# Kernel tuning notes

Hardware: AMD Instinct MI355X
Metric: run time of the kernel (lower is better)

## Reference

```python
import jax, jax.numpy as jnp
import numpy as np
from jax import lax

# --- model constants (match init_kwargs) ---
B = 4096
T, N_FEAT = 100, 81
KH = 7                 # cnn_kernel_height
T_MOD = T - KH + 1     # 94
M = 100                # cnn_hidden_size
P = 128                # decoder hidden size
SKIP = 10
SH = 32                # skip_hidden_size
PT = T_MOD // SKIP     # 9


def setup_inputs() -> dict:
    key = jax.random.key(0)
    ks = jax.random.split(key, 18)
    s = 0.05
    def rn(k, shape, scale=s):
        return jax.random.normal(k, shape, dtype=jnp.float32) * scale
    return {
        "enc_data": jax.random.normal(ks[0], (B, T, N_FEAT), dtype=jnp.float32),
        # Conv2d(1 -> M, kernel=(KH, N_FEAT))
        "conv_w": rn(ks[1], (M, 1, KH, N_FEAT)),
        "conv_b": rn(ks[2], (M,)),
        # TemporalAttention: W_d: Linear(2P->M, no bias), U_d: Linear(M->M, no bias), v_d: Linear(M->1, no bias)
        "Wd": rn(ks[3], (M, 2 * P)),
        "Ud": rn(ks[4], (M, M)),
        "vd": rn(ks[5], (1, M)),
        # LSTM(input=M, hidden=P), PyTorch gate order i,f,g,o
        "lstm_wih": rn(ks[6], (4 * P, M)),
        "lstm_whh": rn(ks[7], (4 * P, P)),
        "lstm_bih": rn(ks[8], (4 * P,)),
        "lstm_bhh": rn(ks[9], (4 * P,)),
        # GRU(input=M, hidden=SH), PyTorch gate order r,z,n
        "gru_wih": rn(ks[10], (3 * SH, M)),
        "gru_whh": rn(ks[11], (3 * SH, SH)),
        "gru_bih": rn(ks[12], (3 * SH,)),
        "gru_bhh": rn(ks[13], (3 * SH,)),
        # output head: Linear(M+P+SKIP*SH -> P), ReLU, (Dropout=eval identity), Linear(P -> 1)
        "out1_w": rn(ks[14], (P, M + P + SKIP * SH)),
        "out1_b": rn(ks[15], (P,)),
        "out2_w": rn(ks[16], (1, P)),
        "out2_b": rn(ks[17], (1,)),
    }


def reference(enc_data, conv_w, conv_b, Wd, Ud, vd,
              lstm_wih, lstm_whh, lstm_bih, lstm_bhh,
              gru_wih, gru_whh, gru_bih, gru_bhh,
              out1_w, out1_b, out2_w, out2_b):
    b = enc_data.shape[0]

    # --- CNN encoder: Conv2d valid over full feature width -> [B, T_MOD, M] ---
    x = enc_data[:, None]  # [B,1,T,n]
    h = lax.conv_general_dilated(x, conv_w, window_strides=(1, 1), padding='VALID',
                                 dimension_numbers=('NCHW', 'OIHW', 'NCHW'))  # [B,M,T_MOD,1]
    H = jax.nn.relu(h + conv_b[None, :, None, None])[..., 0].transpose(0, 2, 1)  # [B,T_MOD,M]

    # precompute U_d(H) once (same math; U_d applied to H is step-invariant)
    HU = jnp.einsum('btm,km->btk', H, Ud)  # [B,T_MOD,M]

    def dec_step(carry, _):
        d, s = carry  # each [B,P]
        q = jnp.concatenate([d, s], axis=1)                       # [B,2P]
        e = jnp.tanh((q @ Wd.T)[:, None, :] + HU)                 # [B,T_MOD,M]
        scores = jnp.einsum('btm,m->bt', e, vd[0])                # [B,T_MOD]
        beta = jax.nn.softmax(scores, axis=1)                     # softmax over time
        c = jnp.einsum('bt,btm->bm', beta, H)                     # context [B,M]
        gates = c @ lstm_wih.T + lstm_bih + d @ lstm_whh.T + lstm_bhh
        i_g, f_g, g_g, o_g = jnp.split(gates, 4, axis=1)
        s_new = jax.nn.sigmoid(f_g) * s + jax.nn.sigmoid(i_g) * jnp.tanh(g_g)
        d_new = jax.nn.sigmoid(o_g) * jnp.tanh(s_new)
        return (d_new, s_new), (beta, c)

    d0 = jnp.zeros((b, P), dtype=enc_data.dtype)
    s0 = jnp.zeros((b, P), dtype=enc_data.dtype)
    (d_T, _), (betas, cs) = lax.scan(dec_step, (d0, s0), None, length=T_MOD)
    c_last = cs[-1]                                               # [B,M]
    dec_out = jnp.concatenate([d_T, c_last], axis=1)              # [B, P+M]

    # --- skip GRU over strided conv features ---
    Hs = H[:, -PT * SKIP:, :]                                     # [B, PT*SKIP, M]
    Hs = (Hs.transpose(0, 2, 1)                                   # [B, M, PT*SKIP]
            .reshape(b, M, PT, SKIP)
            .transpose(2, 0, 3, 1)                                # [PT, B, SKIP, M]
            .reshape(PT, b * SKIP, M))

    def gru_step(hprev, xt):
        gi = xt @ gru_wih.T + gru_bih
        gh = hprev @ gru_whh.T + gru_bhh
        ir, iz, inn = jnp.split(gi, 3, axis=1)
        hr, hz, hn = jnp.split(gh, 3, axis=1)
        r = jax.nn.sigmoid(ir + hr)
        z = jax.nn.sigmoid(iz + hz)
        nn_ = jnp.tanh(inn + r * hn)
        hnew = (1.0 - z) * nn_ + z * hprev
        return hnew, None

    h0 = jnp.zeros((b * SKIP, SH), dtype=enc_data.dtype)
    h_skip, _ = lax.scan(gru_step, h0, Hs)                        # [B*SKIP, SH]
    h_skip = h_skip.reshape(b, SKIP * SH)                         # matches torch view

    feat = jnp.concatenate([dec_out, h_skip], axis=1)             # [B, P+M+SKIP*SH]
    out = jax.nn.relu(feat @ out1_w.T + out1_b) @ out2_w.T + out2_b  # [B,1]
    return out[:, 0]
```

## Files before the change

### kernel.cpp

```cpp
#include <hip/hip_runtime.h>

typedef unsigned int u32;
typedef unsigned short u16;
typedef _Float16 half2_t __attribute__((ext_vector_type(2)));

#define TM 94
#define MD 100
#define DEC_NT 512

__device__ __forceinline__ float bf2f(u16 v){ return __builtin_bit_cast(float, ((u32)v)<<16); }
__device__ __forceinline__ float bflo(u32 v){ return __builtin_bit_cast(float, v<<16); }
__device__ __forceinline__ float bfhi(u32 v){ return __builtin_bit_cast(float, v & 0xffff0000u); }
__device__ __forceinline__ u32 f2bf_bits(float f){ u32 u=__builtin_bit_cast(u32,f); return (u + 0x7fffu + ((u>>16)&1u))>>16; }
__device__ __forceinline__ u32 packbf2(float a, float b){ return f2bf_bits(a) | (f2bf_bits(b)<<16); }
__device__ __forceinline__ u32 packh2(float a, float b){ half2_t h; h.x=(_Float16)a; h.y=(_Float16)b; return __builtin_bit_cast(u32,h); }
__device__ __forceinline__ float fdot2(u32 a, u32 b, float c){
  return __builtin_amdgcn_fdot2(__builtin_bit_cast(half2_t,a), __builtin_bit_cast(half2_t,b), c, false);
}
__device__ __forceinline__ float fast_rcp(float x){ return __builtin_amdgcn_rcpf(x); }
__device__ __forceinline__ float sigmoid_f(float x){ return fast_rcp(1.f + __expf(-x)); }
__device__ __forceinline__ float tanh_f(float x){ float e=__expf(2.f*x); return 1.f - 2.f*fast_rcp(e+1.f); }

__global__ __launch_bounds__(128)
void conv_kernel(const float* __restrict__ enc, const float* __restrict__ cw,
                 const float* __restrict__ cb, u16* __restrict__ Hb)
{
  __shared__ float sE[8100];
  const int tid = threadIdx.x;
  const int b = blockIdx.y;
  const int chunk = blockIdx.x;
  const float* ep = enc + (size_t)b*8100;
  for (int i=tid;i<8100;i+=128) sE[i]=ep[i];
  __syncthreads();
  if (tid >= TM) return;
  const int t = tid;
  const int mo = chunk*10;
  const float* wb = cw + mo*567;
  float acc[10];
  #pragma unroll
  for (int k=0;k<10;k++) acc[k]=cb[mo+k];
  const float* e = sE + t*81;
  #pragma unroll 3
  for (int j=0;j<567;j++){
    float ev = e[j];
    #pragma unroll
    for (int k=0;k<10;k++) acc[k] += ev*wb[k*567+j];
  }
  u32* out = (u32*)Hb + ((size_t)b*9400 + t*100 + mo)/2;
  #pragma unroll
  for (int k=0;k<5;k++) out[k] = packbf2(fmaxf(acc[2*k],0.f), fmaxf(acc[2*k+1],0.f));
}

#define OFF_SHU   37600
#define OFF_SQ    75200
#define OFF_SQ2   77248
#define OFF_SA    78272
#define OFF_SB    79072
#define OFF_SC    79840
#define OFF_SC2   80640
#define OFF_SG    81056
#define OFF_SVD   85152
#define DEC_LDS   85568

__global__ __launch_bounds__(DEC_NT, 2)
void decoder_kernel(const u16* __restrict__ Hb, const float* __restrict__ Wd,
                    const float* __restrict__ Ud, const float* __restrict__ vd,
                    const float* __restrict__ wih, const float* __restrict__ whh,
                    const float* __restrict__ bih, const float* __restrict__ bhh,
                    float* __restrict__ dT, float* __restrict__ cLast)
{
  extern __shared__ char smem[];
  u16*      sH   = (u16*)smem;
  u16*      sHU  = (u16*)(smem + OFF_SHU);
  float*    sq   = (float*)(smem + OFF_SQ);
  _Float16* sq2  = (_Float16*)(smem + OFF_SQ2);
  float*    sa   = (float*)(smem + OFF_SA);
  float*    sbeta= (float*)(smem + OFF_SB);
  float*    sc   = (float*)(smem + OFF_SC);
  _Float16* sc2  = (_Float16*)(smem + OFF_SC2);
  float*    sg   = (float*)(smem + OFF_SG);
  float*    svd  = (float*)(smem + OFF_SVD);

  const int tid = threadIdx.x;
  const int b0 = blockIdx.x * 2;

  {
    const u32* src = (const u32*)(Hb + (size_t)b0*9400);
    u32* dst = (u32*)sH;
    for (int i=tid;i<9400;i+=DEC_NT) dst[i]=src[i];
  }
  if (tid < 100) svd[tid] = vd[tid];
  for (int i=tid;i<512;i+=DEC_NT) sq[i]=0.f;
  {
    u32* q2 = (u32*)sq2;
    for (int i=tid;i<256;i+=DEC_NT) q2[i]=0u;
  }

  u32 Wih[50]; u32 Whh[64]; u32 Wdf[32];
  float biasg;
  {
    const float2* wr = (const float2*)(wih + (size_t)tid*100);
    #pragma unroll
    for (int i=0;i<50;i++){ float2 v = wr[i]; Wih[i]=packh2(v.x,v.y); }
    const float2* hr = (const float2*)(whh + (size_t)tid*128);
    #pragma unroll
    for (int i=0;i<64;i++){ float2 v = hr[i]; Whh[i]=packh2(v.x,v.y); }
    biasg = bih[tid] + bhh[tid];
  }
  const int mw = tid>>2, part = tid&3;
  if (mw < 100){
    const float2* dr = (const float2*)(Wd + mw*256 + part*64);
    #pragma unroll
    for (int i=0;i<32;i++){ float2 v = dr[i]; Wdf[i]=packh2(v.x,v.y); }
  }
  __syncthreads();

  for (int idx=tid; idx<4700; idx+=DEC_NT){
    int kq = idx/188;
    int r  = idx - kq*188;
    int bi = (r>=94)?1:0;
    int t  = r - 94*bi;
    const u32* hrow = (const u32*)sH + bi*4700 + t*50;
    const float* ud0 = Ud + (kq*4+0)*100;
    const float* ud1 = Ud + (kq*4+1)*100;
    const float* ud2 = Ud + (kq*4+2)*100;
    const float* ud3 = Ud + (kq*4+3)*100;
    float c0=0.f,c1=0.f,c2=0.f,c3=0.f;
    #pragma unroll 5
    for (int mq=0; mq<25; mq++){
      u32 h01 = hrow[mq*2], h23 = hrow[mq*2+1];
      float h0=bflo(h01), h1=bfhi(h01), h2=bflo(h23), h3=bfhi(h23);
      float4 u0 = *(const float4*)(ud0 + mq*4);
      float4 u1 = *(const float4*)(ud1 + mq*4);
      float4 u2 = *(const float4*)(ud2 + mq*4);
      float4 u3 = *(const float4*)(ud3 + mq*4);
      c0 += h0*u0.x + h1*u0.y + h2*u0.z + h3*u0.w;
      c1 += h0*u1.x + h1*u1.y + h2*u1.z + h3*u1.w;
      c2 += h0*u2.x + h1*u2.y + h2*u2.z + h3*u2.w;
      c3 += h0*u3.x + h1*u3.y + h2*u3.z + h3*u3.w;
    }
    u32* dst = (u32*)sHU + bi*4700 + t*50 + kq*2;
    dst[0] = packbf2(c0,c1);
    dst[1] = packbf2(c2,c3);
  }
  __syncthreads();

  for (int step=0; step<TM; step++){
    if (mw < 100){
      #pragma unroll
      for (int bi=0;bi<2;bi++){
        const uint4* qp = (const uint4*)((const u32*)sq2 + bi*128 + part*32);
        float a0=0.f, a1=0.f;
        #pragma unroll
        for (int i=0;i<8;i++){
          uint4 qv = qp[i];
          a0 = fdot2(Wdf[4*i+0], qv.x, a0);
          a1 = fdot2(Wdf[4*i+1], qv.y, a1);
          a0 = fdot2(Wdf[4*i+2], qv.z, a0);
          a1 = fdot2(Wdf[4*i+3], qv.w, a1);
        }
        float acc = a0+a1;
        acc += __shfl_xor(acc,1);
        acc += __shfl_xor(acc,2);
        if (part==0) sa[bi*100+mw]=acc;
      }
    }
    __syncthreads();
    if (tid < 376){
      int row = tid>>1, half = tid&1;
      int bi = (row>=94)?1:0;
      int t = row - 94*bi;
      const u16* hu = sHU + bi*9400 + t*100 + half*50;
      const float* ap = sa + bi*100 + half*50;
      const float* vp = svd + half*50;
      float acc=0.f;
      #pragma unroll 5
      for (int m=0;m<50;m++){
        float x = ap[m] + bf2f(hu[m]);
        acc += vp[m]*tanh_f(x);
      }
      acc += __shfl_xor(acc,1);
      if (half==0) sbeta[bi*96+t]=acc;
    }
    __syncthreads();
    if (tid < 128){
      int bi = tid>>6, lane = tid&63;
      float s0 = sbeta[bi*96+lane];
      float s1 = (lane<30)? sbeta[bi*96+64+lane] : -1e30f;
      float mx = fmaxf(s0,s1);
      #pragma unroll
      for (int o=32;o>=1;o>>=1) mx = fmaxf(mx, __shfl_xor(mx,o));
      float e0 = __expf(s0-mx);
      float e1 = (lane<30)? __expf(s1-mx) : 0.f;
      float sm = e0+e1;
      #pragma unroll
      for (int o=32;o>=1;o>>=1) sm += __shfl_xor(sm,o);
      float rs = fast_rcp(sm);
      sbeta[bi*96+lane] = e0*rs;
      if (lane<30) sbeta[bi*96+64+lane] = e1*rs;
    }
    __syncthreads();
    if (tid < 400){
      int bi = (tid>=200)?1:0;
      int rr = tid - 200*bi;
      int m = rr>>1, th = rr&1;
      const float* bp = sbeta + bi*96 + th*47;
      const u16* hp = sH + bi*9400 + th*4700 + m;
      float a0=0.f;
      #pragma unroll
      for (int i=0;i<47;i++) a0 += bp[i]*bf2f(hp[i*100]);
      a0 += __shfl_xor(a0,1);
      if (th==0){
        sc[bi*100+m]=a0;
        sc2[bi*104+m]=(_Float16)a0;
        if (step==TM-1) cLast[(size_t)(b0+bi)*100+m]=a0;
      }
    }
    __syncthreads();
    #pragma unroll
    for (int bi=0;bi<2;bi++){
      float a0 = biasg, a1 = 0.f;
      const uint4* cp = (const uint4*)((const u32*)sc2 + bi*52);
      #pragma unroll
      for (int i=0;i<12;i++){
        uint4 cv = cp[i];
        a0 = fdot2(Wih[4*i+0], cv.x, a0);
        a1 = fdot2(Wih[4*i+1], cv.y, a1);
        a0 = fdot2(Wih[4*i+2], cv.z, a0);
        a1 = fdot2(Wih[4*i+3], cv.w, a1);
      }
      {
        const u32* ct = (const u32*)sc2 + bi*52 + 48;
        a0 = fdot2(Wih[48], ct[0], a0);
        a1 = fdot2(Wih[49], ct[1], a1);
      }
      const uint4* qp = (const uint4*)((const u32*)sq2 + bi*128);
      #pragma unroll
      for (int i=0;i<16;i++){
        uint4 qv = qp[i];
        a0 = fdot2(Whh[4*i+0], qv.x, a0);
        a1 = fdot2(Whh[4*i+1], qv.y, a1);
        a0 = fdot2(Whh[4*i+2], qv.z, a0);
        a1 = fdot2(Whh[4*i+3], qv.w, a1);
      }
      sg[bi*512+tid] = a0+a1;
    }
    __syncthreads();
    if (tid < 256){
      int bi = tid>>7, p = tid&127;
      float ig = sg[bi*512+p];
      float fg = sg[bi*512+128+p];
      float gg = sg[bi*512+256+p];
      float og = sg[bi*512+384+p];
      float s_old = sq[bi*256+128+p];
      float sn = sigmoid_f(fg)*s_old + sigmoid_f(ig)*tanh_f(gg);
      float dn = sigmoid_f(og)*tanh_f(sn);
      sq[bi*256+128+p]=sn; sq[bi*256+p]=dn;
      sq2[bi*256+p]=(_Float16)dn; sq2[bi*256+128+p]=(_Float16)sn;
      if (step==TM-1) dT[(size_t)(b0+bi)*128+p]=dn;
    }
    __syncthreads();
  }
}

__global__ __launch_bounds__(256)
void gru_kernel(const u16* __restrict__ Hb, const float* __restrict__ wih,
                const float* __restrict__ whh, const float* __restrict__ bihp,
                const float* __restrict__ bhhp, float* __restrict__ hskip)
{
  __shared__ float sWih[96][101];
  __shared__ float sWhh[96][33];
  __shared__ float sxt[8][100];
  __shared__ float sh[8][33];
  const int tid = threadIdx.x;
  for (int i=tid;i<9600;i+=256){ sWih[i/100][i%100]=wih[i]; }
  for (int i=tid;i<3072;i+=256){ sWhh[i>>5][i&31]=whh[i]; }
  const int r = tid>>5, j = tid&31;
  const int rowg = blockIdx.x*8 + r;
  const int b = rowg/10, sk = rowg - b*10;
  const float b_r = bihp[j], b_z = bihp[32+j], b_n = bihp[64+j];
  const float hb_r = bhhp[j], hb_z = bhhp[32+j], hb_n = bhhp[64+j];
  sh[r][j]=0.f;
  float h = 0.f;
  __syncthreads();
  for (int pt=0; pt<9; pt++){
    for (int i=tid;i<800;i+=256){
      int rr=i/100, m=i-rr*100;
      int rg = blockIdx.x*8+rr; int bb=rg/10, ss=rg-bb*10;
      sxt[rr][m] = bf2f(Hb[(size_t)bb*9400 + (size_t)(4+pt*10+ss)*100 + m]);
    }
    __syncthreads();
    float gi_r=b_r, gi_z=b_z, gi_n=b_n, gh_r=hb_r, gh_z=hb_z, gh_n=hb_n;
    #pragma unroll 4
    for (int m=0;m<100;m++){
      float x = sxt[r][m];
      gi_r += sWih[j][m]*x; gi_z += sWih[32+j][m]*x; gi_n += sWih[64+j][m]*x;
    }
    #pragma unroll
    for (int k=0;k<32;k++){
      float hp = sh[r][k];
      gh_r += sWhh[j][k]*hp; gh_z += sWhh[32+j][k]*hp; gh_n += sWhh[64+j][k]*hp;
    }
    float rg_ = sigmoid_f(gi_r+gh_r);
    float z  = sigmoid_f(gi_z+gh_z);
    float n  = tanh_f(gi_n + rg_*gh_n);
    h = (1.f-z)*n + z*h;
    __syncthreads();
    sh[r][j]=h;
    __syncthreads();
  }
  hskip[(size_t)b*320 + sk*32 + j] = h;
}

__global__ __launch_bounds__(256)
void out_kernel(const float* __restrict__ dT, const float* __restrict__ cLast,
                const float* __restrict__ hskip, const float* __restrict__ w1,
                const float* __restrict__ b1, const float* __restrict__ w2,
                const float* __restrict__ b2, float* __restrict__ outp)
{
  __shared__ float sf[2][548];
  __shared__ float sred[2][2];
  const int tid = threadIdx.x;
  const int b0 = blockIdx.x*2;
  for (int i=tid;i<2*548;i+=256){
    int bl=i/548, k=i-548*bl; int b=b0+bl;
    float v;
    if (k<128) v = dT[(size_t)b*128+k];
    else if (k<228) v = cLast[(size_t)b*100+(k-128)];
    else v = hskip[(size_t)b*320+(k-228)];
    sf[bl][k]=v;
  }
  __syncthreads();
  const int bl = tid>>7, j = tid&127;
  const float* wr = w1 + (size_t)j*548;
  float acc = b1[j];
  #pragma unroll 4
  for (int k=0;k<548;k++) acc += sf[bl][k]*wr[k];
  float v = fmaxf(acc,0.f)*w2[j];
  #pragma unroll
  for (int o=32;o>=1;o>>=1) v += __shfl_xor(v,o);
  if ((tid&63)==0) sred[bl][j>>6]=v;
  __syncthreads();
  if (j==0) outp[b0+bl] = sred[bl][0]+sred[bl][1]+b2[0];
}

extern "C" void kernel_launch(void* const* d_in, const int* in_sizes, int n_in,
                              void* d_out, int out_size, void* d_ws, size_t ws_size,
                              hipStream_t stream)
{
  const float* enc      = (const float*)d_in[0];
  const float* conv_w   = (const float*)d_in[1];
  const float* conv_b   = (const float*)d_in[2];
  const float* Wd       = (const float*)d_in[3];
  const float* Ud       = (const float*)d_in[4];
  const float* vd       = (const float*)d_in[5];
  const float* lstm_wih = (const float*)d_in[6];
  const float* lstm_whh = (const float*)d_in[7];
  const float* lstm_bih = (const float*)d_in[8];
  const float* lstm_bhh = (const float*)d_in[9];
  const float* gru_wih  = (const float*)d_in[10];
  const float* gru_whh  = (const float*)d_in[11];
  const float* gru_bih  = (const float*)d_in[12];
  const float* gru_bhh  = (const float*)d_in[13];
  const float* out1_w   = (const float*)d_in[14];
  const float* out1_b   = (const float*)d_in[15];
  const float* out2_w   = (const float*)d_in[16];
  const float* out2_b   = (const float*)d_in[17];

  char* ws = (char*)d_ws;
  u16*   Hb    = (u16*)ws;
  float* dT    = (float*)(ws + 77004800);
  float* cLast = (float*)(ws + 79101952);
  float* hskip = (float*)(ws + 80740352);

  conv_kernel<<<dim3(10,4096,1), 128, 0, stream>>>(enc, conv_w, conv_b, Hb);

  (void)hipFuncSetAttribute((const void*)decoder_kernel,
                            hipFuncAttributeMaxDynamicSharedMemorySize, DEC_LDS);
  decoder_kernel<<<2048, DEC_NT, DEC_LDS, stream>>>(Hb, Wd, Ud, vd,
                                                    lstm_wih, lstm_whh, lstm_bih, lstm_bhh,
                                                    dT, cLast);

  gru_kernel<<<5120, 256, 0, stream>>>(Hb, gru_wih, gru_whh, gru_bih, gru_bhh, hskip);

  out_kernel<<<2048, 256, 0, stream>>>(dT, cLast, hskip, out1_w, out1_b, out2_w, out2_b,
                                       (float*)d_out);
}
```

Measured before the change: 8.196 ms.

## Process four batch items per decoder block and tile output head weights in LDS

The decoder kernel now handles four sequences per block instead of two, so the per-thread LSTM and attention weights held in registers are reused across more batch items. Several inner loops are vectorized and rebalanced: full-row tanh scoring per thread, paired context outputs, and rotated Wd reads to spread LDS bank access. Gate values are stored as fp16 and the weight register loads are moved after the Ud precompute. The output head now runs 32 batch items per block with w1 staged through LDS tiles. This raises decoder LDS use to about 163KB, which may cut occupancy to one block per CU, and the fp16 gate storage lowers precision.

```diff
diff --git a/kernel.cpp b/kernel.cpp
--- a/kernel.cpp
+++ b/kernel.cpp
@@ -5,7 +5,7 @@
 typedef _Float16 half2_t __attribute__((ext_vector_type(2)));
 
 #define TM 94
-#define MD 100
+#define NB 4
 #define DEC_NT 512
 
 __device__ __forceinline__ float bf2f(u16 v){ return __builtin_bit_cast(float, ((u32)v)<<16); }
@@ -51,16 +51,15 @@
   for (int k=0;k<5;k++) out[k] = packbf2(fmaxf(acc[2*k],0.f), fmaxf(acc[2*k+1],0.f));
 }
 
-#define OFF_SHU   37600
-#define OFF_SQ    75200
-#define OFF_SQ2   77248
-#define OFF_SA    78272
-#define OFF_SB    79072
-#define OFF_SC    79840
-#define OFF_SC2   80640
-#define OFF_SG    81056
-#define OFF_SVD   85152
-#define DEC_LDS   85568
+#define OFF_SHU   75200
+#define OFF_SQS   150400
+#define OFF_SQ2   152448
+#define OFF_SA    154496
+#define OFF_SB    156096
+#define OFF_SC2   157632
+#define OFF_SG    158464
+#define OFF_SVD   162560
+#define DEC_LDS   162960
 
 __global__ __launch_bounds__(DEC_NT, 2)
 void decoder_kernel(const u16* __restrict__ Hb, const float* __restrict__ Wd,
@@ -72,53 +71,34 @@
   extern __shared__ char smem[];
   u16*      sH   = (u16*)smem;
   u16*      sHU  = (u16*)(smem + OFF_SHU);
-  float*    sq   = (float*)(smem + OFF_SQ);
+  float*    sqs  = (float*)(smem + OFF_SQS);
   _Float16* sq2  = (_Float16*)(smem + OFF_SQ2);
   float*    sa   = (float*)(smem + OFF_SA);
   float*    sbeta= (float*)(smem + OFF_SB);
-  float*    sc   = (float*)(smem + OFF_SC);
-  _Float16* sc2  = (_Float16*)(smem + OFF_SC2);
-  float*    sg   = (float*)(smem + OFF_SG);
+  u32*      sc2  = (u32*)(smem + OFF_SC2);
+  _Float16* sg   = (_Float16*)(smem + OFF_SG);
   float*    svd  = (float*)(smem + OFF_SVD);
 
   const int tid = threadIdx.x;
-  const int b0 = blockIdx.x * 2;
+  const int b0 = blockIdx.x * NB;
 
   {
-    const u32* src = (const u32*)(Hb + (size_t)b0*9400);
-    u32* dst = (u32*)sH;
-    for (int i=tid;i<9400;i+=DEC_NT) dst[i]=src[i];
+    const uint4* src = (const uint4*)(Hb + (size_t)b0*9400);
+    uint4* dst = (uint4*)sH;
+    for (int i=tid;i<4700;i+=DEC_NT) dst[i]=src[i];
   }
   if (tid < 100) svd[tid] = vd[tid];
-  for (int i=tid;i<512;i+=DEC_NT) sq[i]=0.f;
+  for (int i=tid;i<NB*128;i+=DEC_NT) sqs[i]=0.f;
   {
     u32* q2 = (u32*)sq2;
-    for (int i=tid;i<256;i+=DEC_NT) q2[i]=0u;
-  }
-
-  u32 Wih[50]; u32 Whh[64]; u32 Wdf[32];
-  float biasg;
-  {
-    const float2* wr = (const float2*)(wih + (size_t)tid*100);
-    #pragma unroll
-    for (int i=0;i<50;i++){ float2 v = wr[i]; Wih[i]=packh2(v.x,v.y); }
-    const float2* hr = (const float2*)(whh + (size_t)tid*128);
-    #pragma unroll
-    for (int i=0;i<64;i++){ float2 v = hr[i]; Whh[i]=packh2(v.x,v.y); }
-    biasg = bih[tid] + bhh[tid];
-  }
-  const int mw = tid>>2, part = tid&3;
-  if (mw < 100){
-    const float2* dr = (const float2*)(Wd + mw*256 + part*64);
-    #pragma unroll
-    for (int i=0;i<32;i++){ float2 v = dr[i]; Wdf[i]=packh2(v.x,v.y); }
+    for (int i=tid;i<NB*128;i+=DEC_NT) q2[i]=0u;
   }
   __syncthreads();
 
-  for (int idx=tid; idx<4700; idx+=DEC_NT){
-    int kq = idx/188;
-    int r  = idx - kq*188;
-    int bi = (r>=94)?1:0;
+  for (int idx=tid; idx<9400; idx+=DEC_NT){
+    int kq = idx/376;
+    int r  = idx - kq*376;
+    int bi = r/94;
     int t  = r - 94*bi;
     const u32* hrow = (const u32*)sH + bi*4700 + t*50;
     const float* ud0 = Ud + (kq*4+0)*100;
@@ -128,8 +108,8 @@
     float c0=0.f,c1=0.f,c2=0.f,c3=0.f;
     #pragma unroll 5
     for (int mq=0; mq<25; mq++){
-      u32 h01 = hrow[mq*2], h23 = hrow[mq*2+1];
-      float h0=bflo(h01), h1=bfhi(h01), h2=bflo(h23), h3=bfhi(h23);
+      uint2 hp = *(const uint2*)(hrow + mq*2);
+      float h0=bflo(hp.x), h1=bfhi(hp.x), h2=bflo(hp.y), h3=bfhi(hp.y);
       float4 u0 = *(const float4*)(ud0 + mq*4);
       float4 u1 = *(const float4*)(ud1 + mq*4);
       float4 u2 = *(const float4*)(ud2 + mq*4);
@@ -145,19 +125,43 @@
   }
   __syncthreads();
 
+  __builtin_amdgcn_sched_barrier(0);
+  const int mw = tid>>2, part = tid&3;
+  u32 Wih[50]; u32 Whh[64]; u32 Wdf[32];
+  float biasg;
+  {
+    const float2* wr = (const float2*)(wih + (size_t)tid*100);
+    #pragma unroll
+    for (int i=0;i<50;i++){ float2 v = wr[i]; Wih[i]=packh2(v.x,v.y); }
+    const float2* hr = (const float2*)(whh + (size_t)tid*128);
+    #pragma unroll
+    for (int i=0;i<64;i++){ float2 v = hr[i]; Whh[i]=packh2(v.x,v.y); }
+    biasg = bih[tid] + bhh[tid];
+  }
+  if (mw < 100){
+    const float2* dr = (const float2*)(Wd + mw*256 + part*64);
+    #pragma unroll
+    for (int s=0;s<8;s++){
+      int ii = (s+part)&7;
+      #pragma unroll
+      for (int k=0;k<4;k++){ float2 v = dr[ii*4+k]; Wdf[4*s+k]=packh2(v.x,v.y); }
+    }
+  }
+
   for (int step=0; step<TM; step++){
     if (mw < 100){
       #pragma unroll
-      for (int bi=0;bi<2;bi++){
-        const uint4* qp = (const uint4*)((const u32*)sq2 + bi*128 + part*32);
+      for (int bi=0;bi<NB;bi++){
+        const u32* qb = (const u32*)sq2 + bi*128 + part*32;
         float a0=0.f, a1=0.f;
         #pragma unroll
-        for (int i=0;i<8;i++){
-          uint4 qv = qp[i];
-          a0 = fdot2(Wdf[4*i+0], qv.x, a0);
-          a1 = fdot2(Wdf[4*i+1], qv.y, a1);
-          a0 = fdot2(Wdf[4*i+2], qv.z, a0);
-          a1 = fdot2(Wdf[4*i+3], qv.w, a1);
+        for (int s=0;s<8;s++){
+          int ii = (s+part)&7;
+          uint4 qv = *(const uint4*)(qb + ii*4);
+          a0 = fdot2(Wdf[4*s+0], qv.x, a0);
+          a1 = fdot2(Wdf[4*s+1], qv.y, a1);
+          a0 = fdot2(Wdf[4*s+2], qv.z, a0);
+          a1 = fdot2(Wdf[4*s+3], qv.w, a1);
         }
         float acc = a0+a1;
         acc += __shfl_xor(acc,1);
@@ -167,23 +171,38 @@
     }
     __syncthreads();
     if (tid < 376){
-      int row = tid>>1, half = tid&1;
-      int bi = (row>=94)?1:0;
-      int t = row - 94*bi;
-      const u16* hu = sHU + bi*9400 + t*100 + half*50;
-      const float* ap = sa + bi*100 + half*50;
-      const float* vp = svd + half*50;
+      int bi = tid/94;
+      int t  = tid - 94*bi;
+      const u32* hu = (const u32*)sHU + bi*4700 + t*50;
+      const float4* ap4 = (const float4*)(sa + bi*100);
+      const float4* vp4 = (const float4*)svd;
       float acc=0.f;
-      #pragma unroll 5
-      for (int m=0;m<50;m++){
-        float x = ap[m] + bf2f(hu[m]);
-        acc += vp[m]*tanh_f(x);
-      }
-      acc += __shfl_xor(acc,1);
-      if (half==0) sbeta[bi*96+t]=acc;
-    }
-    __syncthreads();
-    if (tid < 128){
+      #pragma unroll
+      for (int c=0;c<12;c++){
+        uint4 h4 = ((const uint4*)hu)[c];
+        float4 a0 = ap4[2*c], a1 = ap4[2*c+1];
+        float4 v0 = vp4[2*c], v1 = vp4[2*c+1];
+        acc += v0.x*tanh_f(a0.x + bflo(h4.x));
+        acc += v0.y*tanh_f(a0.y + bfhi(h4.x));
+        acc += v0.z*tanh_f(a0.z + bflo(h4.y));
+        acc += v0.w*tanh_f(a0.w + bfhi(h4.y));
+        acc += v1.x*tanh_f(a1.x + bflo(h4.z));
+        acc += v1.y*tanh_f(a1.y + bfhi(h4.z));
+        acc += v1.z*tanh_f(a1.z + bflo(h4.w));
+        acc += v1.w*tanh_f(a1.w + bfhi(h4.w));
+      }
+      {
+        uint2 ht = *(const uint2*)(hu + 48);
+        float4 a = ap4[24]; float4 v = vp4[24];
+        acc += v.x*tanh_f(a.x + bflo(ht.x));
+        acc += v.y*tanh_f(a.y + bfhi(ht.x));
+        acc += v.z*tanh_f(a.z + bflo(ht.y));
+        acc += v.w*tanh_f(a.w + bfhi(ht.y));
+      }
+      sbeta[bi*96+t]=acc;
+    }
+    __syncthreads();
+    if (tid < 64*NB){
       int bi = tid>>6, lane = tid&63;
       float s0 = sbeta[bi*96+lane];
       float s1 = (lane<30)? sbeta[bi*96+64+lane] : -1e30f;
@@ -201,26 +220,33 @@
     }
     __syncthreads();
     if (tid < 400){
-      int bi = (tid>=200)?1:0;
-      int rr = tid - 200*bi;
-      int m = rr>>1, th = rr&1;
+      int bi = tid/100;
+      int r  = tid - 100*bi;
+      int mp = r>>1, th = r&1;
       const float* bp = sbeta + bi*96 + th*47;
-      const u16* hp = sH + bi*9400 + th*4700 + m;
-      float a0=0.f;
-      #pragma unroll
-      for (int i=0;i<47;i++) a0 += bp[i]*bf2f(hp[i*100]);
+      const u32* hp = (const u32*)sH + bi*4700 + th*47*50 + mp;
+      float a0=0.f, a1=0.f;
+      #pragma unroll
+      for (int i=0;i<47;i++){
+        float be = bp[i];
+        u32 h = hp[i*50];
+        a0 += be*bflo(h); a1 += be*bfhi(h);
+      }
       a0 += __shfl_xor(a0,1);
+      a1 += __shfl_xor(a1,1);
       if (th==0){
-        sc[bi*100+m]=a0;
-        sc2[bi*104+m]=(_Float16)a0;
-        if (step==TM-1) cLast[(size_t)(b0+bi)*100+m]=a0;
-      }
-    }
-    __syncthreads();
-    #pragma unroll
-    for (int bi=0;bi<2;bi++){
+        sc2[bi*52+mp] = packh2(a0,a1);
+        if (step==TM-1){
+          cLast[(size_t)(b0+bi)*100 + 2*mp]   = a0;
+          cLast[(size_t)(b0+bi)*100 + 2*mp+1] = a1;
+        }
+      }
+    }
+    __syncthreads();
+    #pragma unroll
+    for (int bi=0;bi<NB;bi++){
       float a0 = biasg, a1 = 0.f;
-      const uint4* cp = (const uint4*)((const u32*)sc2 + bi*52);
+      const uint4* cp = (const uint4*)(sc2 + bi*52);
       #pragma unroll
       for (int i=0;i<12;i++){
         uint4 cv = cp[i];
@@ -230,7 +256,7 @@
         a1 = fdot2(Wih[4*i+3], cv.w, a1);
       }
       {
-        const u32* ct = (const u32*)sc2 + bi*52 + 48;
+        const u32* ct = sc2 + bi*52 + 48;
         a0 = fdot2(Wih[48], ct[0], a0);
         a1 = fdot2(Wih[49], ct[1], a1);
       }
@@ -243,20 +269,21 @@
         a0 = fdot2(Whh[4*i+2], qv.z, a0);
         a1 = fdot2(Whh[4*i+3], qv.w, a1);
       }
-      sg[bi*512+tid] = a0+a1;
-    }
-    __syncthreads();
-    if (tid < 256){
+      sg[bi*512+tid] = (_Float16)(a0+a1);
+    }
+    __syncthreads();
+    {
       int bi = tid>>7, p = tid&127;
-      float ig = sg[bi*512+p];
-      float fg = sg[bi*512+128+p];
-      float gg = sg[bi*512+256+p];
-      float og = sg[bi*512+384+p];
-      float s_old = sq[bi*256+128+p];
+      float ig = (float)sg[bi*512+p];
+      float fg = (float)sg[bi*512+128+p];
+      float gg = (float)sg[bi*512+256+p];
+      float og = (float)sg[bi*512+384+p];
+      float s_old = sqs[bi*128+p];
       float sn = sigmoid_f(fg)*s_old + sigmoid_f(ig)*tanh_f(gg);
       float dn = sigmoid_f(og)*tanh_f(sn);
-      sq[bi*256+128+p]=sn; sq[bi*256+p]=dn;
-      sq2[bi*256+p]=(_Float16)dn; sq2[bi*256+128+p]=(_Float16)sn;
+      sqs[bi*128+p]=sn;
+      sq2[bi*256+p]=(_Float16)dn;
+      sq2[bi*256+128+p]=(_Float16)sn;
       if (step==TM-1) dT[(size_t)(b0+bi)*128+p]=dn;
     }
     __syncthreads();
@@ -312,36 +339,48 @@
   hskip[(size_t)b*320 + sk*32 + j] = h;
 }
 
+#define OUT_NB 32
+#define OUT_LDS ((OUT_NB*552 + 8*552)*4)
+
 __global__ __launch_bounds__(256)
 void out_kernel(const float* __restrict__ dT, const float* __restrict__ cLast,
                 const float* __restrict__ hskip, const float* __restrict__ w1,
                 const float* __restrict__ b1, const float* __restrict__ w2,
                 const float* __restrict__ b2, float* __restrict__ outp)
 {
-  __shared__ float sf[2][548];
-  __shared__ float sred[2][2];
+  extern __shared__ float osm[];
+  float* sf = osm;
+  float* sw = osm + OUT_NB*552;
   const int tid = threadIdx.x;
-  const int b0 = blockIdx.x*2;
-  for (int i=tid;i<2*548;i+=256){
-    int bl=i/548, k=i-548*bl; int b=b0+bl;
+  const int b0 = blockIdx.x*OUT_NB;
+  for (int i=tid;i<OUT_NB*548;i+=256){
+    int bl = i/548, k = i - 548*bl; int b = b0+bl;
     float v;
     if (k<128) v = dT[(size_t)b*128+k];
     else if (k<228) v = cLast[(size_t)b*100+(k-128)];
     else v = hskip[(size_t)b*320+(k-228)];
-    sf[bl][k]=v;
-  }
-  __syncthreads();
-  const int bl = tid>>7, j = tid&127;
-  const float* wr = w1 + (size_t)j*548;
-  float acc = b1[j];
-  #pragma unroll 4
-  for (int k=0;k<548;k++) acc += sf[bl][k]*wr[k];
-  float v = fmaxf(acc,0.f)*w2[j];
-  #pragma unroll
-  for (int o=32;o>=1;o>>=1) v += __shfl_xor(v,o);
-  if ((tid&63)==0) sred[bl][j>>6]=v;
-  __syncthreads();
-  if (j==0) outp[b0+bl] = sred[bl][0]+sred[bl][1]+b2[0];
+    sf[bl*552+k]=v;
+  }
+  const int bl = tid>>3, j = tid&7;
+  float outv = 0.f;
+  for (int jt=0; jt<128; jt+=8){
+    __syncthreads();
+    for (int i=tid;i<8*548;i+=256){
+      int rr=i/548, c=i-548*rr;
+      sw[rr*552+c] = w1[(size_t)jt*548 + i];
+    }
+    __syncthreads();
+    float acc = b1[jt+j];
+    const float* fr = sf + bl*552;
+    const float* wr = sw + j*552;
+    #pragma unroll 4
+    for (int k=0;k<548;k++) acc += fr[k]*wr[k];
+    outv += fmaxf(acc,0.f)*w2[jt+j];
+  }
+  outv += __shfl_xor(outv,1);
+  outv += __shfl_xor(outv,2);
+  outv += __shfl_xor(outv,4);
+  if (j==0) outp[b0+bl] = outv + b2[0];
 }
 
 extern "C" void kernel_launch(void* const* d_in, const int* in_sizes, int n_in,
@@ -377,12 +416,14 @@
 
   (void)hipFuncSetAttribute((const void*)decoder_kernel,
                             hipFuncAttributeMaxDynamicSharedMemorySize, DEC_LDS);
-  decoder_kernel<<<2048, DEC_NT, DEC_LDS, stream>>>(Hb, Wd, Ud, vd,
-                                                    lstm_wih, lstm_whh, lstm_bih, lstm_bhh,
-                                                    dT, cLast);
+  decoder_kernel<<<4096/NB, DEC_NT, DEC_LDS, stream>>>(Hb, Wd, Ud, vd,
+                                                       lstm_wih, lstm_whh, lstm_bih, lstm_bhh,
+                                                       dT, cLast);
 
   gru_kernel<<<5120, 256, 0, stream>>>(Hb, gru_wih, gru_whh, gru_bih, gru_bhh, hskip);
 
-  out_kernel<<<2048, 256, 0, stream>>>(dT, cLast, hskip, out1_w, out1_b, out2_w, out2_b,
-                                       (float*)d_out);
-}
+  (void)hipFuncSetAttribute((const void*)out_kernel,
+                            hipFuncAttributeMaxDynamicSharedMemorySize, OUT_LDS);
+  out_kernel<<<4096/OUT_NB, 256, OUT_LDS, stream>>>(dT, cLast, hskip, out1_w, out1_b,
+                                                    out2_w, out2_b, (float*)d_out);
+}
```

New measurement: 7.762 ms. -5.3%, faster.
